# Optimization experiments

Measured on AMD Instinct MI355X. Metric: run time of the kernel, lower is better.

Reference implementation:

```python
import jax, jax.numpy as jnp
import numpy as np

B, D, T = 16384, 1024, 128  # batch, embed_dim, num_degradation_types
V, L = 4, 3                 # variants per sample, degradations per variant


def setup_inputs() -> dict:
    key = jax.random.key(0)
    k1, k2, k3, k4 = jax.random.split(key, 4)
    clean_embeddings = jax.random.normal(k1, (B, D), dtype=jnp.float32)
    W = jax.random.normal(k2, (T, D), dtype=jnp.float32) * (1.0 / np.sqrt(D))
    b = jnp.zeros((T,), dtype=jnp.float32)
    deg_indices = jax.random.randint(k3, (B, V, L), 0, T, dtype=jnp.int32)
    deg_mask = jax.random.randint(k4, (B, V, L), 0, 2, dtype=jnp.int32)
    return {"clean_embeddings": clean_embeddings, "W": W, "b": b,
            "deg_indices": deg_indices, "deg_mask": deg_mask}


def reference(clean_embeddings, W, b, deg_indices, deg_mask):
    # Linear + softmax: [B, T]
    logits = jnp.einsum("bd,td->bt", clean_embeddings, W) + b
    probs = jax.nn.softmax(logits, axis=-1)
    # Gather probs at each (batch, label) pair: [B, V*L] -> [B, V, L]
    flat_idx = deg_indices.reshape(B, V * L)
    gathered = jnp.take_along_axis(probs, flat_idx, axis=1).reshape(B, V, L)
    # Masked sum over all labels of a sample, divided by max(num_variants, 1)=V
    per_sample = (gathered * deg_mask.astype(probs.dtype)).sum(axis=(1, 2)) / V
    return per_sample.sum() / B
```

## Files before the change

kernel.cpp:

```cpp
#include <hip/hip_runtime.h>

#define B_SIZE 16384
#define D_DIM  1024
#define T_DIM  128
#define VLn    12
#define BM     16
#define BK     256
#define NCHUNK 4
#define GRID   (B_SIZE / BM)
#define AROWF  258
#define AROWB  1032
#define ABUFB  (BM * AROWB)
#define SLSTR  132

typedef _Float16 half8  __attribute__((ext_vector_type(8)));
typedef __fp16   fp16x2 __attribute__((ext_vector_type(2)));
typedef float    f32x4  __attribute__((ext_vector_type(4)));

union Pack16 { fp16x2 h[4]; uint4 u; half8 v; };
union Frag   { uint4 u; half8 h; };

__device__ __forceinline__ uint4 pack8u(float4 v0, float4 v1) {
    Pack16 un;
    un.h[0] = __builtin_amdgcn_cvt_pkrtz(v0.x, v0.y);
    un.h[1] = __builtin_amdgcn_cvt_pkrtz(v0.z, v0.w);
    un.h[2] = __builtin_amdgcn_cvt_pkrtz(v1.x, v1.y);
    un.h[3] = __builtin_amdgcn_cvt_pkrtz(v1.z, v1.w);
    return un.u;
}
__device__ __forceinline__ half8 pack8f(const float* fp) {
    const float2 a = ((const float2*)fp)[0];
    const float2 b = ((const float2*)fp)[1];
    const float2 c = ((const float2*)fp)[2];
    const float2 d = ((const float2*)fp)[3];
    Pack16 un;
    un.h[0] = __builtin_amdgcn_cvt_pkrtz(a.x, a.y);
    un.h[1] = __builtin_amdgcn_cvt_pkrtz(b.x, b.y);
    un.h[2] = __builtin_amdgcn_cvt_pkrtz(c.x, c.y);
    un.h[3] = __builtin_amdgcn_cvt_pkrtz(d.x, d.y);
    return un.v;
}

__device__ __forceinline__ void dma16(const float* g, void* l) {
    __builtin_amdgcn_global_load_lds(
        (__attribute__((address_space(1))) void*)g,
        (__attribute__((address_space(3))) void*)l, 16, 0, 0);
}

__global__ __launch_bounds__(256)
void conv_w(const float* __restrict__ W, uint4* __restrict__ Wf) {
    const int j    = blockIdx.x * 256 + threadIdx.x;
    const int kc   = j >> 10;
    const int r    = j & 1023;
    const int g    = r >> 6;
    const int lane = r & 63;
    const int n = (g & 7) * 16 + (lane & 15);
    const int k = kc * 64 + (g >> 3) * 32 + ((lane >> 4) << 3);
    const float* src = W + (size_t)n * D_DIM + k;
    Wf[j] = pack8u(*(const float4*)src, *(const float4*)(src + 4));
}

__global__ __launch_bounds__(256, 2)
void qloss_kernel(const float* __restrict__ emb,
                  const uint4* __restrict__ Wf,
                  const float* __restrict__ bias,
                  const int*   __restrict__ didx,
                  const int*   __restrict__ dmsk,
                  float*       __restrict__ out)
{
    __shared__ __align__(16) unsigned char smem[2 * ABUFB + 16];
    float* sL   = (float*)smem;
    float* sRed = (float*)(smem + 2 * ABUFB);

    const int t    = threadIdx.x;
    const int w    = t >> 6;
    const int lane = t & 63;
    const int m15  = lane & 15;
    const int quad = lane >> 4;
    const int r0   = blockIdx.x * BM;

    const float* aG0 = emb + (size_t)(r0 + 4 * w) * D_DIM + lane * 4;

    const uint4* bP = Wf + lane;
    const int CT0 = 2 * w;

    f32x4 acc[2];
    acc[0] = (f32x4){0.f, 0.f, 0.f, 0.f};
    acc[1] = (f32x4){0.f, 0.f, 0.f, 0.f};

    Frag bc[16], bn[16];

#pragma unroll
    for (int r = 0; r < 4; ++r)
        dma16(aG0 + (size_t)r * D_DIM, smem + (4 * w + r) * AROWB);
#pragma unroll
    for (int ks = 0; ks < 8; ++ks) {
        const int s = ks;
#pragma unroll
        for (int j = 0; j < 2; ++j)
            bc[ks * 2 + j].u = bP[(size_t)(s >> 1) * 1024 + ((s & 1) * 8 + CT0 + j) * 64];
    }
    __syncthreads();

#pragma unroll
    for (int kc = 0; kc < NCHUNK; ++kc) {
        const unsigned char* bufC = smem + (kc & 1) * ABUFB;
        unsigned char*       bufN = (unsigned char*)smem + ((kc & 1) ^ 1) * ABUFB;

        if (kc + 1 < NCHUNK) {
#pragma unroll
            for (int r = 0; r < 4; ++r)
                dma16(aG0 + (size_t)r * D_DIM + (kc + 1) * BK,
                      bufN + (4 * w + r) * AROWB);
#pragma unroll
            for (int ks = 0; ks < 8; ++ks) {
                const int s = (kc + 1) * 8 + ks;
#pragma unroll
                for (int j = 0; j < 2; ++j)
                    bn[ks * 2 + j].u =
                        bP[(size_t)(s >> 1) * 1024 + ((s & 1) * 8 + CT0 + j) * 64];
            }
        }

#pragma unroll
        for (int ks = 0; ks < 8; ++ks) {
            const float* fp = (const float*)bufC + m15 * AROWF + ks * 32 + quad * 8;
            const half8 a = pack8f(fp);
            acc[0] = __builtin_amdgcn_mfma_f32_16x16x32_f16(a, bc[ks * 2 + 0].h, acc[0], 0, 0, 0);
            acc[1] = __builtin_amdgcn_mfma_f32_16x16x32_f16(a, bc[ks * 2 + 1].h, acc[1], 0, 0, 0);
        }
        __syncthreads();

#pragma unroll
        for (int q = 0; q < 16; ++q) bc[q] = bn[q];
    }

    const float b0v = bias[CT0 * 16 + m15];
    const float b1v = bias[(CT0 + 1) * 16 + m15];
#pragma unroll
    for (int i = 0; i < 4; ++i) {
        const int row = quad * 4 + i;
        sL[row * SLSTR + CT0 * 16 + m15]       = acc[0][i] + b0v;
        sL[row * SLSTR + (CT0 + 1) * 16 + m15] = acc[1][i] + b1v;
    }
    __syncthreads();

    {
        const int row = t >> 4, s = t & 15;
        float* base = &sL[row * SLSTR + s * 8];
        float v[8];
        *(float4*)&v[0] = *(const float4*)(base);
        *(float4*)&v[4] = *(const float4*)(base + 4);
        float m = -1e30f;
#pragma unroll
        for (int j = 0; j < 8; ++j) m = fmaxf(m, v[j]);
#pragma unroll
        for (int off = 1; off < 16; off <<= 1) m = fmaxf(m, __shfl_xor(m, off));
        float ssum = 0.f;
#pragma unroll
        for (int j = 0; j < 8; ++j) { v[j] = __expf(v[j] - m); ssum += v[j]; }
#pragma unroll
        for (int off = 1; off < 16; off <<= 1) ssum += __shfl_xor(ssum, off);
        const float inv = 1.0f / ssum;
#pragma unroll
        for (int j = 0; j < 8; ++j) v[j] *= inv;
        *(float4*)(base)     = *(const float4*)&v[0];
        *(float4*)(base + 4) = *(const float4*)&v[4];
    }
    __syncthreads();

    float p = 0.f;
    if (t < BM * VLn) {
        const int gi  = r0 * VLn + t;
        const int row = t / VLn;
        const int idx = didx[gi];
        const int mk  = dmsk[gi];
        p = mk ? sL[row * SLSTR + idx] : 0.f;
    }
#pragma unroll
    for (int off = 1; off < 64; off <<= 1) p += __shfl_xor(p, off);
    if (lane == 0) sRed[w] = p;
    __syncthreads();
    if (t == 0)
        atomicAdd(out, (sRed[0] + sRed[1] + sRed[2] + sRed[3]) * (1.0f / 65536.0f));
}

extern "C" void kernel_launch(void* const* d_in, const int* in_sizes, int n_in,
                              void* d_out, int out_size, void* d_ws, size_t ws_size,
                              hipStream_t stream) {
    const float* emb  = (const float*)d_in[0];
    const float* W    = (const float*)d_in[1];
    const float* bias = (const float*)d_in[2];
    const int*   didx = (const int*)d_in[3];
    const int*   dmsk = (const int*)d_in[4];
    float* out = (float*)d_out;

    uint4* Wf = (uint4*)d_ws;

    hipMemsetAsync(out, 0, sizeof(float), stream);
    conv_w<<<64, 256, 0, stream>>>(W, Wf);
    qloss_kernel<<<GRID, 256, 0, stream>>>(emb, Wf, bias, didx, dmsk, out);
}
```

Before: 114.4 us.

## Give each wave its own 16-row tile with direct global A loads

Restructures the GEMM so each wave owns 16 batch rows and all 128 output columns (8 accumulators). A is loaded straight from global into registers, replacing the LDS DMA staging, block-wide barriers and the cross-wave LDS softmax pass. Softmax now runs in registers on the MFMA accumulators, and each wave does its own gather and atomic add. The output memset is folded into the weight-conversion kernel. In exchange, every wave re-reads all of Wf with no sharing between waves in a block, the A global loads are less coalesced, and the launch bound drops to one block per CU.

```diff
diff --git a/kernel.cpp b/kernel.cpp
--- a/kernel.cpp
+++ b/kernel.cpp
@@ -4,13 +4,6 @@
 #define D_DIM  1024
 #define T_DIM  128
 #define VLn    12
-#define BM     16
-#define BK     256
-#define NCHUNK 4
-#define GRID   (B_SIZE / BM)
-#define AROWF  258
-#define AROWB  1032
-#define ABUFB  (BM * AROWB)
 #define SLSTR  132
 
 typedef _Float16 half8  __attribute__((ext_vector_type(8)));
@@ -28,27 +21,19 @@
     un.h[3] = __builtin_amdgcn_cvt_pkrtz(v1.z, v1.w);
     return un.u;
 }
-__device__ __forceinline__ half8 pack8f(const float* fp) {
-    const float2 a = ((const float2*)fp)[0];
-    const float2 b = ((const float2*)fp)[1];
-    const float2 c = ((const float2*)fp)[2];
-    const float2 d = ((const float2*)fp)[3];
+__device__ __forceinline__ half8 mk8(float4 v0, float4 v1) {
     Pack16 un;
-    un.h[0] = __builtin_amdgcn_cvt_pkrtz(a.x, a.y);
-    un.h[1] = __builtin_amdgcn_cvt_pkrtz(b.x, b.y);
-    un.h[2] = __builtin_amdgcn_cvt_pkrtz(c.x, c.y);
-    un.h[3] = __builtin_amdgcn_cvt_pkrtz(d.x, d.y);
+    un.h[0] = __builtin_amdgcn_cvt_pkrtz(v0.x, v0.y);
+    un.h[1] = __builtin_amdgcn_cvt_pkrtz(v0.z, v0.w);
+    un.h[2] = __builtin_amdgcn_cvt_pkrtz(v1.x, v1.y);
+    un.h[3] = __builtin_amdgcn_cvt_pkrtz(v1.z, v1.w);
     return un.v;
 }
 
-__device__ __forceinline__ void dma16(const float* g, void* l) {
-    __builtin_amdgcn_global_load_lds(
-        (__attribute__((address_space(1))) void*)g,
-        (__attribute__((address_space(3))) void*)l, 16, 0, 0);
-}
-
 __global__ __launch_bounds__(256)
-void conv_w(const float* __restrict__ W, uint4* __restrict__ Wf) {
+void conv_w(const float* __restrict__ W, uint4* __restrict__ Wf,
+            float* __restrict__ out) {
+    if (blockIdx.x == 0 && threadIdx.x == 0) out[0] = 0.0f;
     const int j    = blockIdx.x * 256 + threadIdx.x;
     const int kc   = j >> 10;
     const int r    = j & 1023;
@@ -60,7 +45,7 @@
     Wf[j] = pack8u(*(const float4*)src, *(const float4*)(src + 4));
 }
 
-__global__ __launch_bounds__(256, 2)
+__global__ __launch_bounds__(256, 1)
 void qloss_kernel(const float* __restrict__ emb,
                   const uint4* __restrict__ Wf,
                   const float* __restrict__ bias,
@@ -68,121 +53,92 @@
                   const int*   __restrict__ dmsk,
                   float*       __restrict__ out)
 {
-    __shared__ __align__(16) unsigned char smem[2 * ABUFB + 16];
-    float* sL   = (float*)smem;
-    float* sRed = (float*)(smem + 2 * ABUFB);
+    __shared__ float sP[4][16 * SLSTR];
 
     const int t    = threadIdx.x;
     const int w    = t >> 6;
     const int lane = t & 63;
     const int m15  = lane & 15;
     const int quad = lane >> 4;
-    const int r0   = blockIdx.x * BM;
+    const int r0   = blockIdx.x * 64 + w * 16;
 
-    const float* aG0 = emb + (size_t)(r0 + 4 * w) * D_DIM + lane * 4;
+    const float* aP = emb + (size_t)(r0 + m15) * D_DIM + quad * 8;
+    const uint4* bQ = Wf + lane;
 
-    const uint4* bP = Wf + lane;
-    const int CT0 = 2 * w;
+    f32x4 acc[8];
+#pragma unroll
+    for (int ct = 0; ct < 8; ++ct) acc[ct] = (f32x4){0.f, 0.f, 0.f, 0.f};
 
-    f32x4 acc[2];
-    acc[0] = (f32x4){0.f, 0.f, 0.f, 0.f};
-    acc[1] = (f32x4){0.f, 0.f, 0.f, 0.f};
+    Frag bc[8], bn[8];
+    float4 a0c, a1c, a0n, a1n;
 
-    Frag bc[16], bn[16];
+    a0c = *(const float4*)(aP);
+    a1c = *(const float4*)(aP + 4);
+#pragma unroll
+    for (int ct = 0; ct < 8; ++ct) bc[ct].u = bQ[ct * 64];
 
+#pragma unroll 2
+    for (int s = 0; s < 32; ++s) {
+        if (s + 1 < 32) {
+            a0n = *(const float4*)(aP + (s + 1) * 32);
+            a1n = *(const float4*)(aP + (s + 1) * 32 + 4);
 #pragma unroll
-    for (int r = 0; r < 4; ++r)
-        dma16(aG0 + (size_t)r * D_DIM, smem + (4 * w + r) * AROWB);
+            for (int ct = 0; ct < 8; ++ct)
+                bn[ct].u = bQ[(s + 1) * 512 + ct * 64];
+        }
+        const half8 a = mk8(a0c, a1c);
 #pragma unroll
-    for (int ks = 0; ks < 8; ++ks) {
-        const int s = ks;
+        for (int ct = 0; ct < 8; ++ct)
+            acc[ct] = __builtin_amdgcn_mfma_f32_16x16x32_f16(a, bc[ct].h, acc[ct], 0, 0, 0);
+        a0c = a0n; a1c = a1n;
 #pragma unroll
-        for (int j = 0; j < 2; ++j)
-            bc[ks * 2 + j].u = bP[(size_t)(s >> 1) * 1024 + ((s & 1) * 8 + CT0 + j) * 64];
-    }
-    __syncthreads();
-
-#pragma unroll
-    for (int kc = 0; kc < NCHUNK; ++kc) {
-        const unsigned char* bufC = smem + (kc & 1) * ABUFB;
-        unsigned char*       bufN = (unsigned char*)smem + ((kc & 1) ^ 1) * ABUFB;
-
-        if (kc + 1 < NCHUNK) {
-#pragma unroll
-            for (int r = 0; r < 4; ++r)
-                dma16(aG0 + (size_t)r * D_DIM + (kc + 1) * BK,
-                      bufN + (4 * w + r) * AROWB);
-#pragma unroll
-            for (int ks = 0; ks < 8; ++ks) {
-                const int s = (kc + 1) * 8 + ks;
-#pragma unroll
-                for (int j = 0; j < 2; ++j)
-                    bn[ks * 2 + j].u =
-                        bP[(size_t)(s >> 1) * 1024 + ((s & 1) * 8 + CT0 + j) * 64];
-            }
-        }
-
-#pragma unroll
-        for (int ks = 0; ks < 8; ++ks) {
-            const float* fp = (const float*)bufC + m15 * AROWF + ks * 32 + quad * 8;
-            const half8 a = pack8f(fp);
-            acc[0] = __builtin_amdgcn_mfma_f32_16x16x32_f16(a, bc[ks * 2 + 0].h, acc[0], 0, 0, 0);
-            acc[1] = __builtin_amdgcn_mfma_f32_16x16x32_f16(a, bc[ks * 2 + 1].h, acc[1], 0, 0, 0);
-        }
-        __syncthreads();
-
-#pragma unroll
-        for (int q = 0; q < 16; ++q) bc[q] = bn[q];
+        for (int ct = 0; ct < 8; ++ct) bc[ct] = bn[ct];
     }
 
-    const float b0v = bias[CT0 * 16 + m15];
-    const float b1v = bias[(CT0 + 1) * 16 + m15];
+    float bv[8];
+#pragma unroll
+    for (int ct = 0; ct < 8; ++ct) bv[ct] = bias[ct * 16 + m15];
+
 #pragma unroll
     for (int i = 0; i < 4; ++i) {
         const int row = quad * 4 + i;
-        sL[row * SLSTR + CT0 * 16 + m15]       = acc[0][i] + b0v;
-        sL[row * SLSTR + (CT0 + 1) * 16 + m15] = acc[1][i] + b1v;
+        float mx = -1e30f;
+#pragma unroll
+        for (int ct = 0; ct < 8; ++ct) {
+            acc[ct][i] += bv[ct];
+            mx = fmaxf(mx, acc[ct][i]);
+        }
+#pragma unroll
+        for (int off = 1; off < 16; off <<= 1) mx = fmaxf(mx, __shfl_xor(mx, off));
+        float ss = 0.f;
+#pragma unroll
+        for (int ct = 0; ct < 8; ++ct) {
+            const float e = __expf(acc[ct][i] - mx);
+            acc[ct][i] = e;
+            ss += e;
+        }
+#pragma unroll
+        for (int off = 1; off < 16; off <<= 1) ss += __shfl_xor(ss, off);
+        const float inv = 1.0f / ss;
+#pragma unroll
+        for (int ct = 0; ct < 8; ++ct)
+            sP[w][row * SLSTR + ct * 16 + m15] = acc[ct][i] * inv;
     }
-    __syncthreads();
-
-    {
-        const int row = t >> 4, s = t & 15;
-        float* base = &sL[row * SLSTR + s * 8];
-        float v[8];
-        *(float4*)&v[0] = *(const float4*)(base);
-        *(float4*)&v[4] = *(const float4*)(base + 4);
-        float m = -1e30f;
-#pragma unroll
-        for (int j = 0; j < 8; ++j) m = fmaxf(m, v[j]);
-#pragma unroll
-        for (int off = 1; off < 16; off <<= 1) m = fmaxf(m, __shfl_xor(m, off));
-        float ssum = 0.f;
-#pragma unroll
-        for (int j = 0; j < 8; ++j) { v[j] = __expf(v[j] - m); ssum += v[j]; }
-#pragma unroll
-        for (int off = 1; off < 16; off <<= 1) ssum += __shfl_xor(ssum, off);
-        const float inv = 1.0f / ssum;
-#pragma unroll
-        for (int j = 0; j < 8; ++j) v[j] *= inv;
-        *(float4*)(base)     = *(const float4*)&v[0];
-        *(float4*)(base + 4) = *(const float4*)&v[4];
-    }
-    __syncthreads();
 
     float p = 0.f;
-    if (t < BM * VLn) {
-        const int gi  = r0 * VLn + t;
-        const int row = t / VLn;
-        const int idx = didx[gi];
-        const int mk  = dmsk[gi];
-        p = mk ? sL[row * SLSTR + idx] : 0.f;
+#pragma unroll
+    for (int e = 0; e < 3; ++e) {
+        const int item = e * 64 + lane;
+        const int row  = item / VLn;
+        const int j    = item - row * VLn;
+        const int gi   = (r0 + row) * VLn + j;
+        const int mk   = dmsk[gi];
+        const int idx  = didx[gi];
+        if (mk) p += sP[w][row * SLSTR + idx];
     }
 #pragma unroll
     for (int off = 1; off < 64; off <<= 1) p += __shfl_xor(p, off);
-    if (lane == 0) sRed[w] = p;
-    __syncthreads();
-    if (t == 0)
-        atomicAdd(out, (sRed[0] + sRed[1] + sRed[2] + sRed[3]) * (1.0f / 65536.0f));
+    if (lane == 0) atomicAdd(out, p * (1.0f / 65536.0f));
 }
 
 extern "C" void kernel_launch(void* const* d_in, const int* in_sizes, int n_in,
@@ -197,7 +153,6 @@
 
     uint4* Wf = (uint4*)d_ws;
 
-    hipMemsetAsync(out, 0, sizeof(float), stream);
-    conv_w<<<64, 256, 0, stream>>>(W, Wf);
-    qloss_kernel<<<GRID, 256, 0, stream>>>(emb, Wf, bias, didx, dmsk, out);
+    conv_w<<<64, 256, 0, stream>>>(W, Wf, out);
+    qloss_kernel<<<B_SIZE / 64, 256, 0, stream>>>(emb, Wf, bias, didx, dmsk, out);
 }
```

Result: slower. 129.8 us (+13.4%).
